# Performance work log

Hardware: AMD Instinct MI355X
Metric: run time of the kernel (lower is better)

## Reference

```python
import jax, jax.numpy as jnp
import numpy as np

N, E = 50000, 800000
IN, HID, HEADS = 64, 32, 4


def setup_inputs() -> dict:
    key = jax.random.key(0)
    ks = jax.random.split(key, 18)
    x = jax.random.normal(ks[0], (N, IN), jnp.float32)
    edge_index = jax.random.randint(ks[1], (2, E), 0, N)

    def lin(k, fan_in, fan_out):
        kw, kb = jax.random.split(k)
        bound = 1.0 / np.sqrt(fan_in)
        W = jax.random.uniform(kw, (fan_in, fan_out), jnp.float32, -bound, bound)
        b = jax.random.uniform(kb, (fan_out,), jnp.float32, -bound, bound)
        return W, b

    # layer 1: in=IN, out=HID per head, heads=HEADS, concat=True -> out dim HID*HEADS
    Wq1, bq1 = lin(ks[2], IN, HEADS * HID)
    Wk1, bk1 = lin(ks[3], IN, HEADS * HID)
    Wv1, bv1 = lin(ks[4], IN, HEADS * HID)
    Ws1, bs1 = lin(ks[5], IN, HEADS * HID)  # root/skip lin
    # layer 2: in=HID*HEADS, out=HID, heads=1, concat=False
    IN2 = HID * HEADS
    Wq2, bq2 = lin(ks[6], IN2, HID)
    Wk2, bk2 = lin(ks[7], IN2, HID)
    Wv2, bv2 = lin(ks[8], IN2, HID)
    Ws2, bs2 = lin(ks[9], IN2, HID)
    return dict(x=x, edge_index=edge_index,
                Wq1=Wq1, bq1=bq1, Wk1=Wk1, bk1=bk1, Wv1=Wv1, bv1=bv1, Ws1=Ws1, bs1=bs1,
                Wq2=Wq2, bq2=bq2, Wk2=Wk2, bk2=bk2, Wv2=Wv2, bv2=bv2, Ws2=Ws2, bs2=bs2)


def transformer_conv(x, src, dst, Wq, bq, Wk, bk, Wv, bv, Ws, bs, heads, out_ch, concat):
    """PyG TransformerConv (eval mode, root_weight=True, beta=False)."""
    n = x.shape[0]
    q = (x @ Wq + bq).reshape(n, heads, out_ch)  # [N,H,C]
    k = (x @ Wk + bk).reshape(n, heads, out_ch)
    v = (x @ Wv + bv).reshape(n, heads, out_ch)
    # per-edge attention logits: q_i . k_j / sqrt(C)
    logits = jnp.einsum('ehc,ehc->eh', q[dst], k[src]) / jnp.sqrt(jnp.float32(out_ch))
    # segment softmax over incoming edges of each target node
    m = jax.ops.segment_max(logits, dst, num_segments=n)          # [N,H]
    p = jnp.exp(logits - m[dst])                                   # [E,H]
    denom = jax.ops.segment_sum(p, dst, num_segments=n)            # [N,H]
    alpha = p / denom[dst]                                         # [E,H]
    agg = jax.ops.segment_sum(alpha[:, :, None] * v[src], dst, num_segments=n)  # [N,H,C]
    if concat:
        o = agg.reshape(n, heads * out_ch)
    else:
        o = agg.mean(axis=1)
    return o + x @ Ws + bs


def reference(x, edge_index,
              Wq1, bq1, Wk1, bk1, Wv1, bv1, Ws1, bs1,
              Wq2, bq2, Wk2, bk2, Wv2, bv2, Ws2, bs2):
    src, dst = edge_index[0], edge_index[1]
    h = transformer_conv(x, src, dst, Wq1, bq1, Wk1, bk1, Wv1, bv1, Ws1, bs1,
                         HEADS, HID, True)
    h = jax.nn.elu(h)
    out = transformer_conv(h, src, dst, Wq2, bq2, Wk2, bk2, Wv2, bv2, Ws2, bs2,
                           1, HID, False)
    return out
```

## Files before the change

### kernel.cpp

```cpp
#include <hip/hip_runtime.h>
#include <hip/hip_bf16.h>

#define N_NODES 50000
#define N_EDGES 800000
#define HB 3125
#define GB1 1563

static constexpr float SCALE = 0.17677669529663687f;

typedef __attribute__((ext_vector_type(8))) short bf16x8;
typedef __attribute__((ext_vector_type(4))) float f32x4;
#define MFMA16 __builtin_amdgcn_mfma_f32_16x16x32_bf16

static __device__ inline unsigned short f2bf(float f) {
    __hip_bfloat16 h = __float2bfloat16(f);
    return __builtin_bit_cast(unsigned short, h);
}
static __device__ inline float2 bfpair(unsigned u) {
    return make_float2(__uint_as_float(u << 16),
                       __uint_as_float(u & 0xffff0000u));
}
static __device__ inline float dot8(const float* q, uint4 u) {
    float2 a = bfpair(u.x), b = bfpair(u.y), c = bfpair(u.z), d = bfpair(u.w);
    return q[0]*a.x + q[1]*a.y + q[2]*b.x + q[3]*b.y
         + q[4]*c.x + q[5]*c.y + q[6]*d.x + q[7]*d.y;
}
static __device__ inline void acc8(float* acc, float w, uint4 u) {
    float2 a = bfpair(u.x), b = bfpair(u.y), c = bfpair(u.z), d = bfpair(u.w);
    acc[0] += w*a.x; acc[1] += w*a.y; acc[2] += w*b.x; acc[3] += w*b.y;
    acc[4] += w*c.x; acc[5] += w*c.y; acc[6] += w*d.x; acc[7] += w*d.y;
}
static __device__ inline void unpack8(float* o, uint4 u) {
    float2 a = bfpair(u.x), b = bfpair(u.y), c = bfpair(u.z), d = bfpair(u.w);
    o[0]=a.x; o[1]=a.y; o[2]=b.x; o[3]=b.y; o[4]=c.x; o[5]=c.y; o[6]=d.x; o[7]=d.y;
}
static __device__ inline bf16x8 cvt8(const float* p) {
    float4 f0 = *(const float4*)p;
    float4 f1 = *(const float4*)(p + 4);
    bf16x8 r;
    r[0] = (short)f2bf(f0.x); r[1] = (short)f2bf(f0.y);
    r[2] = (short)f2bf(f0.z); r[3] = (short)f2bf(f0.w);
    r[4] = (short)f2bf(f1.x); r[5] = (short)f2bf(f1.y);
    r[6] = (short)f2bf(f1.z); r[7] = (short)f2bf(f1.w);
    return r;
}


__global__ __launch_bounds__(256) void k_heads(
    const int* __restrict__ dst, int* __restrict__ cnt, int* __restrict__ rank,
    const float* __restrict__ Wq1, const float* __restrict__ Wk1,
    const float* __restrict__ Wv1, const float* __restrict__ Ws1,
    const float* __restrict__ Wq2, const float* __restrict__ Wk2,
    const float* __restrict__ Wv2, const float* __restrict__ Ws2,
    unsigned short* __restrict__ Wf1, unsigned short* __restrict__ Wf2)
{
    if (blockIdx.x < HB) {
        int e = blockIdx.x * 256 + threadIdx.x;
        rank[e] = atomicAdd(&cnt[dst[e]], 1);
        return;
    }
    int id = (blockIdx.x - HB) * 256 + threadIdx.x;
    if (id < 32768) {
        int j = id & 7, l = (id >> 3) & 63, ks = (id >> 9) & 1, nt = (id >> 10) & 7, m = (id >> 13) & 3;
        const float* W = (m == 0) ? Wq1 : (m == 1) ? Wk1 : (m == 2) ? Wv1 : Ws1;
        int k = ks * 32 + ((l >> 4) << 3) + j;
        int c = nt * 16 + (l & 15);
        Wf1[id] = f2bf(W[k * 128 + c]);
    } else if (id < 49152) {
        int id2 = id - 32768;
        int j = id2 & 7, l = (id2 >> 3) & 63, ks = (id2 >> 9) & 3, g = (id2 >> 11) & 7;
        int m = g >> 1, t = g & 1;
        const float* W = (m == 0) ? Wq2 : (m == 1) ? Wk2 : (m == 2) ? Wv2 : Ws2;
        int k = ks * 32 + ((l >> 4) << 3) + j;
        int c = t * 16 + (l & 15);
        Wf2[id2] = f2bf(W[k * 32 + c]);
    }
}


__global__ __launch_bounds__(256) void k_scan1(const int* __restrict__ cnt,
                                               int* __restrict__ row,
                                               int* __restrict__ bsum, int n) {
    __shared__ int wsum[4];
    int t = threadIdx.x;
    int base = blockIdx.x * 1024 + t * 4;
    int v0 = (base + 0 < n) ? cnt[base + 0] : 0;
    int v1 = (base + 1 < n) ? cnt[base + 1] : 0;
    int v2 = (base + 2 < n) ? cnt[base + 2] : 0;
    int v3 = (base + 3 < n) ? cnt[base + 3] : 0;
    int s = v0 + v1 + v2 + v3;
    int lane = t & 63, wid = t >> 6;
    int sc = s;
#pragma unroll
    for (int d = 1; d < 64; d <<= 1) {
        int o = __shfl_up(sc, d);
        if (lane >= d) sc += o;
    }
    if (lane == 63) wsum[wid] = sc;
    __syncthreads();
    int woff = 0;
    for (int w = 0; w < wid; ++w) woff += wsum[w];
    int excl = woff + sc - s;
    if (base + 0 < n) row[base + 0] = excl;
    if (base + 1 < n) row[base + 1] = excl + v0;
    if (base + 2 < n) row[base + 2] = excl + v0 + v1;
    if (base + 3 < n) row[base + 3] = excl + v0 + v1 + v2;
    if (t == 255) bsum[blockIdx.x] = woff + sc;
}

__global__ void k_scan2(const int* __restrict__ bsum, int* __restrict__ boff,
                        int* __restrict__ row, int nb) {
    int t = threadIdx.x;
    int v = (t < nb) ? bsum[t] : 0;
    int sc = v;
#pragma unroll
    for (int d = 1; d < 64; d <<= 1) {
        int o = __shfl_up(sc, d);
        if (t >= d) sc += o;
    }
    boff[t] = sc - v;
    if (t == (N_NODES >> 10)) row[N_NODES] = N_EDGES - (sc - v);
}


__global__ __launch_bounds__(256) void k_work(
    const int* __restrict__ src, const int* __restrict__ dst,
    const int* __restrict__ row, const int* __restrict__ boff,
    const int* __restrict__ rank, int* __restrict__ col,
    const float* __restrict__ x, const unsigned short* __restrict__ Wf1,
    const float* __restrict__ bq, const float* __restrict__ bk,
    const float* __restrict__ bv, const float* __restrict__ bs,
    unsigned short* __restrict__ qs1, unsigned short* __restrict__ kv1, int n)
{
    if (blockIdx.x < HB) {
        int e = blockIdx.x * 256 + threadIdx.x;
        int de = dst[e];
        col[row[de] + boff[de >> 10] + rank[e]] = src[e];
        return;
    }
    int w = threadIdx.x >> 6;
    int l = threadIdx.x & 63;
    int rb = (blockIdx.x - HB) * 32;
    int lr = l & 15, lk = l >> 4;
    f32x4 acc[2][8];
#pragma unroll
    for (int mt = 0; mt < 2; ++mt)
#pragma unroll
        for (int nt = 0; nt < 8; ++nt) acc[mt][nt] = (f32x4){0.f, 0.f, 0.f, 0.f};
#pragma unroll
    for (int ks = 0; ks < 2; ++ks) {
        bf16x8 a[2];
#pragma unroll
        for (int mt = 0; mt < 2; ++mt) {
            int r = rb + mt * 16 + lr;
            if (r >= n) r = n - 1;
            a[mt] = cvt8(x + (size_t)r * 64 + ks * 32 + lk * 8);
        }
#pragma unroll
        for (int nt = 0; nt < 8; ++nt) {
            bf16x8 b = *(const bf16x8*)(Wf1 + (size_t)((w * 8 + nt) * 1024 + ks * 512 + l * 8));
            acc[0][nt] = MFMA16(a[0], b, acc[0][nt], 0, 0, 0);
            acc[1][nt] = MFMA16(a[1], b, acc[1][nt], 0, 0, 0);
        }
    }
    const float* bptr = (w == 0) ? bq : (w == 1) ? bk : (w == 2) ? bv : bs;
    unsigned short* outp = (w == 0) ? qs1 : (w == 3) ? qs1 + 128 : (w == 1) ? kv1 : kv1 + 128;
#pragma unroll
    for (int nt = 0; nt < 8; ++nt) {
        int c = nt * 16 + lr;
        float bias = bptr[c];
#pragma unroll
        for (int mt = 0; mt < 2; ++mt) {
#pragma unroll
            for (int i = 0; i < 4; ++i) {
                int r = rb + mt * 16 + lk * 4 + i;
                if (r < n)
                    outp[(size_t)r * 256 + c] = f2bf(acc[mt][nt][i] + bias);
            }
        }
    }
}


__global__ __launch_bounds__(256) void k_gemm2m(
    const unsigned short* __restrict__ h1b, const unsigned short* __restrict__ Wf2,
    const float* __restrict__ bq, const float* __restrict__ bk,
    const float* __restrict__ bv, const float* __restrict__ bs,
    unsigned short* __restrict__ qs2, unsigned short* __restrict__ kv2, int n)
{
    int w = threadIdx.x >> 6;
    int l = threadIdx.x & 63;
    int half = w & 1;
    int rb = blockIdx.x * 64 + (w >> 1) * 32;
    int lr = l & 15, lk = l >> 4;
    f32x4 acc[2][4];
#pragma unroll
    for (int mt = 0; mt < 2; ++mt)
#pragma unroll
        for (int nt = 0; nt < 4; ++nt) acc[mt][nt] = (f32x4){0.f, 0.f, 0.f, 0.f};
#pragma unroll
    for (int ks = 0; ks < 4; ++ks) {
        bf16x8 a[2];
#pragma unroll
        for (int mt = 0; mt < 2; ++mt) {
            int r = rb + mt * 16 + lr;
            if (r >= n) r = n - 1;
            a[mt] = *(const bf16x8*)(h1b + (size_t)r * 128 + ks * 32 + lk * 8);
        }
#pragma unroll
        for (int nt = 0; nt < 4; ++nt) {
            int g = half * 4 + nt;
            bf16x8 b = *(const bf16x8*)(Wf2 + (size_t)((g * 4 + ks) * 512 + l * 8));
            acc[0][nt] = MFMA16(a[0], b, acc[0][nt], 0, 0, 0);
            acc[1][nt] = MFMA16(a[1], b, acc[1][nt], 0, 0, 0);
        }
    }
#pragma unroll
    for (int nt = 0; nt < 4; ++nt) {
        int g = half * 4 + nt;
        int mat = g >> 1;
        int c = (g * 16 + lr) & 31;
        const float* bp = (mat == 0) ? bq : (mat == 1) ? bk : (mat == 2) ? bv : bs;
        unsigned short* outp = (mat == 0) ? qs2 : (mat == 3) ? qs2 + 32
                             : (mat == 1) ? kv2 : kv2 + 32;
        float bias = bp[c];
#pragma unroll
        for (int mt = 0; mt < 2; ++mt) {
#pragma unroll
            for (int i = 0; i < 4; ++i) {
                int r = rb + mt * 16 + lk * 4 + i;
                if (r < n)
                    outp[(size_t)r * 64 + c] = f2bf(acc[mt][nt][i] + bias);
            }
        }
    }
}


__global__ __launch_bounds__(256) void k_agg1(
    const unsigned short* __restrict__ qs1, const unsigned short* __restrict__ kv1,
    const int* __restrict__ row, const int* __restrict__ boff,
    const int* __restrict__ col, uint4* __restrict__ h1b, int n)
{
    int i = blockIdx.x * 4 + (threadIdx.x >> 6);
    if (i >= n) return;
    int lane = threadIdx.x & 63;
    int slot = lane >> 4, w = lane & 15;
    float q[8];
    unpack8(q, *(const uint4*)(qs1 + (size_t)i * 256 + w * 8));
    float acc[8] = {};
    float d = 0.f;
    int s = row[i] + boff[i >> 10];
    int e = row[i + 1] + boff[(i + 1) >> 10];
    for (int t = s; t < e; t += 8) {
        int ta = t + slot, tb = t + 4 + slot;
        bool va = ta < e, vb = tb < e;
        int ja = col[va ? ta : s];
        int jb = col[vb ? tb : s];
        const unsigned short* pa = kv1 + (size_t)ja * 256;
        const unsigned short* pb = kv1 + (size_t)jb * 256;
        uint4 ka = *(const uint4*)(pa + w * 8);
        uint4 kb = *(const uint4*)(pb + w * 8);
        uint4 vA = *(const uint4*)(pa + 128 + w * 8);
        uint4 vB = *(const uint4*)(pb + 128 + w * 8);
        float la = dot8(q, ka);
        float lb = dot8(q, kb);
        la += __shfl_xor(la, 1);  lb += __shfl_xor(lb, 1);
        la += __shfl_xor(la, 2);  lb += __shfl_xor(lb, 2);
        float wa = va ? __expf(la * SCALE) : 0.f;
        float wb = vb ? __expf(lb * SCALE) : 0.f;
        d += wa + wb;
        acc8(acc, wa, vA);
        acc8(acc, wb, vB);
    }
#pragma unroll
    for (int m = 16; m <= 32; m <<= 1) {
        d += __shfl_xor(d, m);
#pragma unroll
        for (int c = 0; c < 8; ++c) acc[c] += __shfl_xor(acc[c], m);
    }
    if (slot == 0) {
        float inv = (d > 0.f) ? 1.f / d : 0.f;
        float sv[8];
        unpack8(sv, *(const uint4*)(qs1 + (size_t)i * 256 + 128 + w * 8));
        unsigned o[4];
#pragma unroll
        for (int p = 0; p < 4; ++p) {
            float rx = acc[2 * p] * inv + sv[2 * p];
            float ry = acc[2 * p + 1] * inv + sv[2 * p + 1];
            rx = (rx > 0.f) ? rx : expm1f(rx);
            ry = (ry > 0.f) ? ry : expm1f(ry);
            o[p] = ((unsigned)f2bf(ry) << 16) | (unsigned)f2bf(rx);
        }
        h1b[(size_t)i * 16 + w] = make_uint4(o[0], o[1], o[2], o[3]);
    }
}


__global__ __launch_bounds__(256) void k_agg2(
    const unsigned short* __restrict__ qs2, const unsigned short* __restrict__ kv2,
    const int* __restrict__ row, const int* __restrict__ boff,
    const int* __restrict__ col, float* __restrict__ out, int n)
{
    int i = blockIdx.x * 4 + (threadIdx.x >> 6);
    if (i >= n) return;
    int lane = threadIdx.x & 63;
    int slot = lane >> 2, qr = lane & 3;
    float q[8];
    unpack8(q, *(const uint4*)(qs2 + (size_t)i * 64 + qr * 8));
    float acc[8] = {};
    float d = 0.f;
    int s = row[i] + boff[i >> 10];
    int e = row[i + 1] + boff[(i + 1) >> 10];
    for (int t = s; t < e; t += 16) {
        int te = t + slot;
        bool va = te < e;
        int j = col[va ? te : s];
        const unsigned short* p = kv2 + (size_t)j * 64;
        uint4 ku = *(const uint4*)(p + qr * 8);
        uint4 vu = *(const uint4*)(p + 32 + qr * 8);
        float lg = dot8(q, ku);
        lg += __shfl_xor(lg, 1);
        lg += __shfl_xor(lg, 2);
        float wv = va ? __expf(lg * SCALE) : 0.f;
        d += wv;
        acc8(acc, wv, vu);
    }
#pragma unroll
    for (int m = 4; m <= 32; m <<= 1) {
        d += __shfl_xor(d, m);
#pragma unroll
        for (int c = 0; c < 8; ++c) acc[c] += __shfl_xor(acc[c], m);
    }
    if (slot == 0) {
        float inv = (d > 0.f) ? 1.f / d : 0.f;
        float sv[8];
        unpack8(sv, *(const uint4*)(qs2 + (size_t)i * 64 + 32 + qr * 8));
        float4 o0, o1;
        o0.x = acc[0] * inv + sv[0];
        o0.y = acc[1] * inv + sv[1];
        o0.z = acc[2] * inv + sv[2];
        o0.w = acc[3] * inv + sv[3];
        o1.x = acc[4] * inv + sv[4];
        o1.y = acc[5] * inv + sv[5];
        o1.z = acc[6] * inv + sv[6];
        o1.w = acc[7] * inv + sv[7];
        *(float4*)&out[(size_t)i * 32 + qr * 8] = o0;
        *(float4*)&out[(size_t)i * 32 + qr * 8 + 4] = o1;
    }
}


extern "C" void kernel_launch(void* const* d_in, const int* in_sizes, int n_in,
                              void* d_out, int out_size, void* d_ws, size_t ws_size,
                              hipStream_t stream)
{
    const int N = N_NODES, E = N_EDGES;
    const float* x   = (const float*)d_in[0];
    const int* edge  = (const int*)d_in[1];
    const int* src   = edge;
    const int* dst   = edge + E;
    const float* Wq1 = (const float*)d_in[2];  const float* bq1 = (const float*)d_in[3];
    const float* Wk1 = (const float*)d_in[4];  const float* bk1 = (const float*)d_in[5];
    const float* Wv1 = (const float*)d_in[6];  const float* bv1 = (const float*)d_in[7];
    const float* Ws1 = (const float*)d_in[8];  const float* bs1 = (const float*)d_in[9];
    const float* Wq2 = (const float*)d_in[10]; const float* bq2 = (const float*)d_in[11];
    const float* Wk2 = (const float*)d_in[12]; const float* bk2 = (const float*)d_in[13];
    const float* Wv2 = (const float*)d_in[14]; const float* bv2 = (const float*)d_in[15];
    const float* Ws2 = (const float*)d_in[16]; const float* bs2 = (const float*)d_in[17];

    char* ws = (char*)d_ws;
    size_t off = 0;
    auto alloc = [&](size_t bytes) -> void* {
        void* p = ws + off;
        off += (bytes + 255) & ~(size_t)255;
        return p;
    };
    unsigned short* qs1 = (unsigned short*)alloc((size_t)N * 256 * 2);
    unsigned short* kv1 = (unsigned short*)alloc((size_t)N * 256 * 2);
    unsigned short* h1b = (unsigned short*)alloc((size_t)N * 128 * 2);
    unsigned short* qs2 = (unsigned short*)alloc((size_t)N * 64 * 2);
    unsigned short* kv2 = (unsigned short*)alloc((size_t)N * 64 * 2);
    unsigned short* Wf1 = (unsigned short*)alloc(32768 * 2);
    unsigned short* Wf2 = (unsigned short*)alloc(16384 * 2);
    int* row_ptr  = (int*)alloc((size_t)(N + 1) * 4);
    int* cnt      = (int*)alloc((size_t)N * 4);
    int* rank     = (int*)alloc((size_t)E * 4);
    int* colb     = (int*)alloc((size_t)E * 4);
    int* bsum     = (int*)alloc(64 * 4);
    int* boff     = (int*)alloc(64 * 4);

    int NBS = (N + 1023) / 1024;

    hipMemsetAsync(cnt, 0, (size_t)N * 4, stream);
    k_heads<<<HB + 192, 256, 0, stream>>>(dst, cnt, rank,
                                          Wq1, Wk1, Wv1, Ws1, Wq2, Wk2, Wv2, Ws2,
                                          Wf1, Wf2);
    k_scan1<<<NBS, 256, 0, stream>>>(cnt, row_ptr, bsum, N);
    k_scan2<<<1, 64, 0, stream>>>(bsum, boff, row_ptr, NBS);
    k_work<<<HB + GB1, 256, 0, stream>>>(src, dst, row_ptr, boff, rank, colb,
                                         x, Wf1, bq1, bk1, bv1, bs1, qs1, kv1, N);
    k_agg1<<<(N + 3) / 4, 256, 0, stream>>>(qs1, kv1, row_ptr, boff, colb, (uint4*)h1b, N);
    k_gemm2m<<<(N + 63) / 64, 256, 0, stream>>>(h1b, Wf2, bq2, bk2, bv2, bs2, qs2, kv2, N);
    k_agg2<<<(N + 3) / 4, 256, 0, stream>>>(qs2, kv2, row_ptr, boff, colb, (float*)d_out, N);
}
```

Baseline: 188.0 us.

## Store layer-1 keys in FP8 and merge scan kernels via last-block pattern

Layer-1 keys are now written as FP8 e4m3 into a separate compact buffer, and values go to their own bf16 buffer. This halves the key bytes gathered per edge in the first aggregation, and the dot product uses hardware packed FP8-to-float conversion. Separately, the two prefix-scan launches are fused into one kernel, where the last block to finish, detected with an atomic counter, scans the block sums. FP8 keys lower the precision of the attention logits, which may push results past the tolerance.

```diff
diff --git a/kernel.cpp b/kernel.cpp
--- a/kernel.cpp
+++ b/kernel.cpp
@@ -1,24 +1,39 @@
 #include <hip/hip_runtime.h>
 #include <hip/hip_bf16.h>
+#include <hip/hip_fp8.h>
 
 #define N_NODES 50000
 #define N_EDGES 800000
 #define HB 3125
 #define GB1 1563
+#define NBS 49
 
 static constexpr float SCALE = 0.17677669529663687f;
 
 typedef __attribute__((ext_vector_type(8))) short bf16x8;
 typedef __attribute__((ext_vector_type(4))) float f32x4;
+typedef __attribute__((ext_vector_type(2))) float f32x2;
 #define MFMA16 __builtin_amdgcn_mfma_f32_16x16x32_bf16
 
 static __device__ inline unsigned short f2bf(float f) {
     __hip_bfloat16 h = __float2bfloat16(f);
     return __builtin_bit_cast(unsigned short, h);
 }
+static __device__ inline unsigned char f2fp8(float f) {
+    __hip_fp8_e4m3 h(f);
+    return __builtin_bit_cast(unsigned char, h);
+}
 static __device__ inline float2 bfpair(unsigned u) {
     return make_float2(__uint_as_float(u << 16),
                        __uint_as_float(u & 0xffff0000u));
+}
+static __device__ inline float dot8f8(const float* q, uint2 u) {
+    f32x2 a = __builtin_amdgcn_cvt_pk_f32_fp8(u.x, false);
+    f32x2 b = __builtin_amdgcn_cvt_pk_f32_fp8(u.x, true);
+    f32x2 c = __builtin_amdgcn_cvt_pk_f32_fp8(u.y, false);
+    f32x2 d = __builtin_amdgcn_cvt_pk_f32_fp8(u.y, true);
+    return q[0]*a[0] + q[1]*a[1] + q[2]*b[0] + q[3]*b[1]
+         + q[4]*c[0] + q[5]*c[1] + q[6]*d[0] + q[7]*d[1];
 }
 static __device__ inline float dot8(const float* q, uint4 u) {
     float2 a = bfpair(u.x), b = bfpair(u.y), c = bfpair(u.z), d = bfpair(u.w);
@@ -78,10 +93,13 @@
 }
 
 
-__global__ __launch_bounds__(256) void k_scan1(const int* __restrict__ cnt,
-                                               int* __restrict__ row,
-                                               int* __restrict__ bsum, int n) {
+__global__ __launch_bounds__(256) void k_scan(const int* __restrict__ cnt,
+                                              int* __restrict__ row,
+                                              int* __restrict__ bsum,
+                                              int* __restrict__ boff,
+                                              int* __restrict__ ctr, int n) {
     __shared__ int wsum[4];
+    __shared__ int lastBlk;
     int t = threadIdx.x;
     int base = blockIdx.x * 1024 + t * 4;
     int v0 = (base + 0 < n) ? cnt[base + 0] : 0;
@@ -105,21 +123,24 @@
     if (base + 1 < n) row[base + 1] = excl + v0;
     if (base + 2 < n) row[base + 2] = excl + v0 + v1;
     if (base + 3 < n) row[base + 3] = excl + v0 + v1 + v2;
-    if (t == 255) bsum[blockIdx.x] = woff + sc;
-}
-
-__global__ void k_scan2(const int* __restrict__ bsum, int* __restrict__ boff,
-                        int* __restrict__ row, int nb) {
-    int t = threadIdx.x;
-    int v = (t < nb) ? bsum[t] : 0;
-    int sc = v;
-#pragma unroll
-    for (int d = 1; d < 64; d <<= 1) {
-        int o = __shfl_up(sc, d);
-        if (t >= d) sc += o;
-    }
-    boff[t] = sc - v;
-    if (t == (N_NODES >> 10)) row[N_NODES] = N_EDGES - (sc - v);
+    if (t == 255) {
+        bsum[blockIdx.x] = woff + sc;
+        __threadfence();
+        lastBlk = (atomicAdd(ctr, 1) == (int)gridDim.x - 1);
+    }
+    __syncthreads();
+    if (lastBlk && t < 64) {
+        __threadfence();
+        int v = (t < NBS) ? ((volatile int*)bsum)[t] : 0;
+        int sc2 = v;
+#pragma unroll
+        for (int d = 1; d < 64; d <<= 1) {
+            int o = __shfl_up(sc2, d);
+            if (t >= d) sc2 += o;
+        }
+        boff[t] = sc2 - v;
+        if (t == (N_NODES >> 10)) row[N_NODES] = N_EDGES - (sc2 - v);
+    }
 }
 
 
@@ -130,7 +151,8 @@
     const float* __restrict__ x, const unsigned short* __restrict__ Wf1,
     const float* __restrict__ bq, const float* __restrict__ bk,
     const float* __restrict__ bv, const float* __restrict__ bs,
-    unsigned short* __restrict__ qs1, unsigned short* __restrict__ kv1, int n)
+    unsigned short* __restrict__ qs1, unsigned char* __restrict__ k8,
+    unsigned short* __restrict__ v1, int n)
 {
     if (blockIdx.x < HB) {
         int e = blockIdx.x * 256 + threadIdx.x;
@@ -164,19 +186,33 @@
         }
     }
     const float* bptr = (w == 0) ? bq : (w == 1) ? bk : (w == 2) ? bv : bs;
-    unsigned short* outp = (w == 0) ? qs1 : (w == 3) ? qs1 + 128 : (w == 1) ? kv1 : kv1 + 128;
-#pragma unroll
-    for (int nt = 0; nt < 8; ++nt) {
-        int c = nt * 16 + lr;
-        float bias = bptr[c];
-#pragma unroll
-        for (int mt = 0; mt < 2; ++mt) {
-#pragma unroll
-            for (int i = 0; i < 4; ++i) {
-                int r = rb + mt * 16 + lk * 4 + i;
-                if (r < n)
-                    outp[(size_t)r * 256 + c] = f2bf(acc[mt][nt][i] + bias);
-            }
+    if (w == 1) {
+#pragma unroll
+        for (int nt = 0; nt < 8; ++nt) {
+            int c = nt * 16 + lr;
+            float bias = bptr[c];
+#pragma unroll
+            for (int mt = 0; mt < 2; ++mt)
+#pragma unroll
+                for (int i = 0; i < 4; ++i) {
+                    int r = rb + mt * 16 + lk * 4 + i;
+                    if (r < n) k8[(size_t)r * 128 + c] = f2fp8(acc[mt][nt][i] + bias);
+                }
+        }
+    } else {
+        unsigned short* outp = (w == 0) ? qs1 : (w == 3) ? qs1 + 128 : v1;
+        size_t stride = (w == 2) ? 128 : 256;
+#pragma unroll
+        for (int nt = 0; nt < 8; ++nt) {
+            int c = nt * 16 + lr;
+            float bias = bptr[c];
+#pragma unroll
+            for (int mt = 0; mt < 2; ++mt)
+#pragma unroll
+                for (int i = 0; i < 4; ++i) {
+                    int r = rb + mt * 16 + lk * 4 + i;
+                    if (r < n) outp[(size_t)r * stride + c] = f2bf(acc[mt][nt][i] + bias);
+                }
         }
     }
 }
@@ -238,7 +274,8 @@
 
 
 __global__ __launch_bounds__(256) void k_agg1(
-    const unsigned short* __restrict__ qs1, const unsigned short* __restrict__ kv1,
+    const unsigned short* __restrict__ qs1, const unsigned char* __restrict__ k8,
+    const unsigned short* __restrict__ v1,
     const int* __restrict__ row, const int* __restrict__ boff,
     const int* __restrict__ col, uint4* __restrict__ h1b, int n)
 {
@@ -257,14 +294,12 @@
         bool va = ta < e, vb = tb < e;
         int ja = col[va ? ta : s];
         int jb = col[vb ? tb : s];
-        const unsigned short* pa = kv1 + (size_t)ja * 256;
-        const unsigned short* pb = kv1 + (size_t)jb * 256;
-        uint4 ka = *(const uint4*)(pa + w * 8);
-        uint4 kb = *(const uint4*)(pb + w * 8);
-        uint4 vA = *(const uint4*)(pa + 128 + w * 8);
-        uint4 vB = *(const uint4*)(pb + 128 + w * 8);
-        float la = dot8(q, ka);
-        float lb = dot8(q, kb);
+        uint2 ka = *(const uint2*)(k8 + (size_t)ja * 128 + w * 8);
+        uint2 kb = *(const uint2*)(k8 + (size_t)jb * 128 + w * 8);
+        uint4 vA = *(const uint4*)(v1 + (size_t)ja * 128 + w * 8);
+        uint4 vB = *(const uint4*)(v1 + (size_t)jb * 128 + w * 8);
+        float la = dot8f8(q, ka);
+        float lb = dot8f8(q, kb);
         la += __shfl_xor(la, 1);  lb += __shfl_xor(lb, 1);
         la += __shfl_xor(la, 2);  lb += __shfl_xor(lb, 2);
         float wa = va ? __expf(la * SCALE) : 0.f;
@@ -377,30 +412,29 @@
         return p;
     };
     unsigned short* qs1 = (unsigned short*)alloc((size_t)N * 256 * 2);
-    unsigned short* kv1 = (unsigned short*)alloc((size_t)N * 256 * 2);
+    unsigned char*  k8  = (unsigned char*)alloc((size_t)N * 128);
+    unsigned short* v1  = (unsigned short*)alloc((size_t)N * 128 * 2);
     unsigned short* h1b = (unsigned short*)alloc((size_t)N * 128 * 2);
     unsigned short* qs2 = (unsigned short*)alloc((size_t)N * 64 * 2);
     unsigned short* kv2 = (unsigned short*)alloc((size_t)N * 64 * 2);
     unsigned short* Wf1 = (unsigned short*)alloc(32768 * 2);
     unsigned short* Wf2 = (unsigned short*)alloc(16384 * 2);
     int* row_ptr  = (int*)alloc((size_t)(N + 1) * 4);
-    int* cnt      = (int*)alloc((size_t)N * 4);
+    int* cnt      = (int*)alloc((size_t)(N + 64) * 4);
+    int* ctr      = cnt + N;
     int* rank     = (int*)alloc((size_t)E * 4);
     int* colb     = (int*)alloc((size_t)E * 4);
     int* bsum     = (int*)alloc(64 * 4);
     int* boff     = (int*)alloc(64 * 4);
 
-    int NBS = (N + 1023) / 1024;
-
-    hipMemsetAsync(cnt, 0, (size_t)N * 4, stream);
+    hipMemsetAsync(cnt, 0, (size_t)(N + 64) * 4, stream);
     k_heads<<<HB + 192, 256, 0, stream>>>(dst, cnt, rank,
                                           Wq1, Wk1, Wv1, Ws1, Wq2, Wk2, Wv2, Ws2,
                                           Wf1, Wf2);
-    k_scan1<<<NBS, 256, 0, stream>>>(cnt, row_ptr, bsum, N);
-    k_scan2<<<1, 64, 0, stream>>>(bsum, boff, row_ptr, NBS);
+    k_scan<<<NBS, 256, 0, stream>>>(cnt, row_ptr, bsum, boff, ctr, N);
     k_work<<<HB + GB1, 256, 0, stream>>>(src, dst, row_ptr, boff, rank, colb,
-                                         x, Wf1, bq1, bk1, bv1, bs1, qs1, kv1, N);
-    k_agg1<<<(N + 3) / 4, 256, 0, stream>>>(qs1, kv1, row_ptr, boff, colb, (uint4*)h1b, N);
+                                         x, Wf1, bq1, bk1, bv1, bs1, qs1, k8, v1, N);
+    k_agg1<<<(N + 3) / 4, 256, 0, stream>>>(qs1, k8, v1, row_ptr, boff, colb, (uint4*)h1b, N);
     k_gemm2m<<<(N + 63) / 64, 256, 0, stream>>>(h1b, Wf2, bq2, bk2, bv2, bs2, qs2, kv2, N);
     k_agg2<<<(N + 3) / 4, 256, 0, stream>>>(qs2, kv2, row_ptr, boff, colb, (float*)d_out, N);
 }
```

New measurement: 183.5 us. 1.02x faster.
